# Optimization experiments

Hardware: AMD Instinct MI355X
Metric: run time of the kernel (lower is better)

Reference implementation:

```python
import jax, jax.numpy as jnp
import numpy as np

IN_DIM = 256
OUT_DIM = 256
B, N, E = 8, 1024, 262144
K_RATIO = 0.5
BN_EPS = 1e-5


def _xavier(key, shape):
    fan_in, fan_out = shape[1], shape[0]
    lim = float(np.sqrt(6.0 / (fan_in + fan_out)))
    return jax.random.uniform(key, shape, jnp.float32, -lim, lim)


def setup_inputs() -> dict:
    key = jax.random.key(0)
    ks = jax.random.split(key, 10)
    x = jax.random.normal(ks[0], (B, N, IN_DIM), jnp.float32)
    edges = jax.random.randint(ks[1], (2, E), 0, B * N, jnp.int64 if jax.config.jax_enable_x64 else jnp.int32)
    return {
        "x": x,
        "edges": edges,
        "att_proj_w": _xavier(ks[2], (OUT_DIM, IN_DIM)),
        "att_proj_b": jnp.zeros((OUT_DIM,), jnp.float32),
        "att_map_w": _xavier(ks[3], (1, OUT_DIM)).reshape(OUT_DIM),
        "pwa_w": _xavier(ks[4], (OUT_DIM, IN_DIM)),
        "pwa_b": jnp.zeros((OUT_DIM,), jnp.float32),
        "pwo_w": _xavier(ks[5], (OUT_DIM, IN_DIM)),
        "pwo_b": jnp.zeros((OUT_DIM,), jnp.float32),
        "bn_gamma": jnp.ones((OUT_DIM,), jnp.float32),
        "bn_beta": jnp.zeros((OUT_DIM,), jnp.float32),
        "y_w": _xavier(ks[6], (1, OUT_DIM)).reshape(OUT_DIM),
        "y_b": jnp.zeros((), jnp.float32),
    }


def reference(x, edges, att_proj_w, att_proj_b, att_map_w, pwa_w, pwa_b,
              pwo_w, pwo_b, bn_gamma, bn_beta, y_w, y_b):
    b, n, d = x.shape
    num_nodes = b * n
    xf = x.reshape(num_nodes, d)
    src, dst = edges[0], edges[1]  # x_j = source, x_i = destination

    # --- GAT message: alpha = att_map(tanh(att_proj(x_i * x_j))) ---
    x_j = xf[src]                                # [E, d]
    x_i = xf[dst]                                # [E, d]
    h = jnp.tanh((x_i * x_j) @ att_proj_w.T + att_proj_b)  # [E, out]
    alpha = h @ att_map_w                        # [E]

    # --- segment softmax over destination nodes ---
    amax = jax.ops.segment_max(alpha, dst, num_segments=num_nodes)
    a = jnp.exp(alpha - amax[dst])
    denom = jax.ops.segment_sum(a, dst, num_segments=num_nodes)
    w = a / (denom[dst] + 1e-16)

    # --- scatter-sum aggregate of alpha * x_j ---
    agg = jax.ops.segment_sum(w[:, None] * x_j, dst, num_segments=num_nodes)  # [num_nodes, d]

    out = agg @ pwa_w.T + pwa_b + xf @ pwo_w.T + pwo_b  # [num_nodes, out]

    # --- BatchNorm1d (training-mode batch stats, biased var) + SELU ---
    mean = out.mean(axis=0)
    var = out.var(axis=0)
    out = (out - mean) * jax.lax.rsqrt(var + BN_EPS) * bn_gamma + bn_beta
    out = jax.nn.selu(out)

    out = out.reshape(b, n, -1)  # [B, N, out]

    # --- GraphPool: top-k by sigmoid score, gate by score ---
    y = jax.nn.sigmoid(out @ y_w + y_b)  # [B, N]
    k = max(int(n * K_RATIO), 1)
    vals, ids = jax.lax.top_k(y, k)      # [B, k]
    x_top = jnp.take_along_axis(out, ids[..., None], axis=1)  # [B, k, out]
    return x_top * vals[..., None]
```

## Files before the change

### kernel.cpp

```cpp
#include <hip/hip_runtime.h>
#include <math.h>

#define NODES 8192
#define NEDGE 262144
#define DIM 256

typedef float f32x16 __attribute__((ext_vector_type(16)));
typedef _Float16 f16x8 __attribute__((ext_vector_type(8)));
typedef __fp16 h16x2 __attribute__((ext_vector_type(2)));
typedef unsigned short u16;
typedef u16 u16x8 __attribute__((ext_vector_type(8)));
typedef u16 u16x4 __attribute__((ext_vector_type(4)));

__device__ __forceinline__ float fast_tanh(float x) {
    float t = __expf(2.f * x);
    return 1.f - 2.f * __builtin_amdgcn_rcpf(t + 1.f);
}

__device__ __forceinline__ u16 h_bits(_Float16 h) {
    u16 r; __builtin_memcpy(&r, &h, 2); return r;
}

union SplitU { h16x2 h2[2]; u16x4 u4; };

__device__ __forceinline__ void split4(float p0, float p1, float p2, float p3,
                                       u16x4& v1, u16x4& v2) {
    h16x2 h01 = __builtin_amdgcn_cvt_pkrtz(p0, p1);
    h16x2 h23 = __builtin_amdgcn_cvt_pkrtz(p2, p3);
    h16x2 r01 = __builtin_amdgcn_cvt_pkrtz((p0 - (float)h01[0]) * 2048.f,
                                           (p1 - (float)h01[1]) * 2048.f);
    h16x2 r23 = __builtin_amdgcn_cvt_pkrtz((p2 - (float)h23[0]) * 2048.f,
                                           (p3 - (float)h23[1]) * 2048.f);
    SplitU c1, c2;
    c1.h2[0] = h01; c1.h2[1] = h23;
    c2.h2[0] = r01; c2.h2[1] = r23;
    v1 = c1.u4; v2 = c2.u4;
}

__global__ void k_deg(const int* __restrict__ dst, int* __restrict__ deg) {
    int e = blockIdx.x * blockDim.x + threadIdx.x;
    if (e < NEDGE) atomicAdd(&deg[dst[e]], 1);
}

__global__ void k_scan(const int* __restrict__ deg, int* __restrict__ rowptr,
                       int* __restrict__ cursor) {
    __shared__ int part[256];
    int t = threadIdx.x;
    int base = t * 32;
    int local[32];
    int s = 0;
    for (int i = 0; i < 32; ++i) { local[i] = s; s += deg[base + i]; }
    part[t] = s;
    __syncthreads();
    for (int off = 1; off < 256; off <<= 1) {
        int v = (t >= off) ? part[t - off] : 0;
        __syncthreads();
        part[t] += v;
        __syncthreads();
    }
    int excl = (t == 0) ? 0 : part[t - 1];
    for (int i = 0; i < 32; ++i) {
        int v = excl + local[i];
        rowptr[base + i] = v;
        cursor[base + i] = v;
    }
    if (t == 255) rowptr[NODES] = part[255];
}

__global__ void k_fill(const int* __restrict__ src, const int* __restrict__ dst,
                       int* __restrict__ cursor, int2* __restrict__ sdg) {
    int e = blockIdx.x * blockDim.x + threadIdx.x;
    if (e < NEDGE) {
        int pos = atomicAdd(&cursor[dst[e]], 1);
        sdg[pos] = make_int2(src[e], dst[e]);
    }
}

__global__ void k_wfrag_all(const float* __restrict__ W, const float* __restrict__ Wa,
                            const float* __restrict__ Wo, u16* __restrict__ wf,
                            u16* __restrict__ wf2) {
    int t = blockIdx.x * blockDim.x + threadIdx.x;
    const float* S;
    u16* D;
    int gks, w, mt, lane;
    if (t < 8192) {
        lane = t & 63; mt = (t >> 6) & 1; w = (t >> 7) & 3; gks = t >> 9;
        S = W; D = wf;
    } else {
        int t2 = t - 8192;
        if (t2 >= 16384) return;
        lane = t2 & 63; mt = (t2 >> 6) & 1; w = (t2 >> 7) & 3; gks = t2 >> 9;
        S = (gks < 16) ? Wa : Wo; D = wf2;
    }
    int row = w * 64 + mt * 32 + (lane & 31);
    int k0 = (gks & 15) * 16 + (lane >> 5) * 8;
    const float* p = S + (size_t)row * DIM + k0;
    u16x8 v1, v2;
#pragma unroll
    for (int j = 0; j < 8; ++j) {
        float f = p[j];
        _Float16 h1 = (_Float16)f;
        _Float16 h2 = (_Float16)((f - (float)h1) * 2048.f);
        v1[j] = h_bits(h1);
        v2[j] = h_bits(h2);
    }
    size_t base = ((size_t)(gks * 4 + w) * 4 + mt * 2) * 512 + lane * 8;
    *(u16x8*)(D + base)       = v1;
    *(u16x8*)(D + base + 512) = v2;
}

__global__ __launch_bounds__(256, 2) void k_alpha_v15(
    const float* __restrict__ x, const int2* __restrict__ sdg,
    const u16* __restrict__ wf, const float* __restrict__ bias,
    const float* __restrict__ amap, float* __restrict__ alpha_pos)
{
    __shared__ u16 p_lds[2][64][256];
    const int tid = threadIdx.x;
    const int w = tid >> 6;
    const int lane = tid & 63;
    const int l31 = lane & 31;
    const int g2 = lane >> 5;
    const int bid = blockIdx.x;
    const int wg = (bid & 7) * 512 + (bid >> 3);
    const int e0 = wg * 64;
    const int ebase = e0 + w * 16;
    const unsigned swz = ((unsigned)(l31 & 7)) << 4;

    f32x16 accM[2][2], accC[2][2];
#pragma unroll
    for (int mt = 0; mt < 2; ++mt)
#pragma unroll
        for (int nt = 0; nt < 2; ++nt) { accM[mt][nt] = (f32x16)0.f; accC[mt][nt] = (f32x16)0.f; }

    f16x8 afA[2][2], afB[2][2], afC[2][2];

#define PREFA(DST, GKS) { \
    const u16* pb_ = wf + ((size_t)((GKS) * 4 + w) * 4) * 512 + lane * 8; \
    _Pragma("unroll") for (int mt_ = 0; mt_ < 2; ++mt_) \
    _Pragma("unroll") for (int pl_ = 0; pl_ < 2; ++pl_) \
        DST[mt_][pl_] = *(const f16x8*)(const void*)(pb_ + (mt_ * 2 + pl_) * 512); }

#define KS(GKS, USE, PF) { \
    if ((GKS) + 2 < 16) { PREFA(PF, (GKS) + 2) } \
    f16x8 bfr[2][2]; \
    _Pragma("unroll") for (int nt_ = 0; nt_ < 2; ++nt_) { \
        const int en_ = nt_ * 32 + l31; \
        const unsigned off_ = ((unsigned)((GKS) * 32 + g2 * 16)) ^ swz; \
        _Pragma("unroll") for (int pl_ = 0; pl_ < 2; ++pl_) \
            bfr[nt_][pl_] = *(const f16x8*)(const void*)((const char*)&p_lds[pl_][en_][0] + off_); \
    } \
    _Pragma("unroll") for (int mt_ = 0; mt_ < 2; ++mt_) \
    _Pragma("unroll") for (int nt_ = 0; nt_ < 2; ++nt_) { \
        accM[mt_][nt_] = __builtin_amdgcn_mfma_f32_32x32x16_f16(USE[mt_][0], bfr[nt_][0], accM[mt_][nt_], 0, 0, 0); \
        accC[mt_][nt_] = __builtin_amdgcn_mfma_f32_32x32x16_f16(USE[mt_][0], bfr[nt_][1], accC[mt_][nt_], 0, 0, 0); \
        accC[mt_][nt_] = __builtin_amdgcn_mfma_f32_32x32x16_f16(USE[mt_][1], bfr[nt_][0], accC[mt_][nt_], 0, 0, 0); } }

    PREFA(afA, 0)
    PREFA(afB, 1)

#pragma unroll
    for (int i = 0; i < 16; ++i) {
        int2 sd = sdg[ebase + i];
        float4 a = *(const float4*)(x + (size_t)sd.x * DIM + lane * 4);
        float4 b = *(const float4*)(x + (size_t)sd.y * DIM + lane * 4);
        u16x4 v1, v2;
        split4(a.x * b.x, a.y * b.y, a.z * b.z, a.w * b.w, v1, v2);
        const int le = w * 16 + i;
        const unsigned off = ((unsigned)(lane * 8)) ^ (((unsigned)(le & 7)) << 4);
        *(u16x4*)((char*)&p_lds[0][le][0] + off) = v1;
        *(u16x4*)((char*)&p_lds[1][le][0] + off) = v2;
    }
    __syncthreads();

    KS(0,  afA, afC) KS(1,  afB, afA) KS(2,  afC, afB)
    KS(3,  afA, afC) KS(4,  afB, afA) KS(5,  afC, afB)
    KS(6,  afA, afC) KS(7,  afB, afA) KS(8,  afC, afB)
    KS(9,  afA, afC) KS(10, afB, afA) KS(11, afC, afB)
    KS(12, afA, afC) KS(13, afB, afA) KS(14, afC, afB)
    KS(15, afA, afC)
#undef KS
#undef PREFA

    float part[2] = {0.f, 0.f};
#pragma unroll
    for (int mt = 0; mt < 2; ++mt)
#pragma unroll
        for (int r = 0; r < 16; ++r) {
            int o = 64 * w + 32 * mt + (r & 3) + 8 * (r >> 2) + 4 * g2;
            float bo = bias[o], ao = amap[o];
#pragma unroll
            for (int nt = 0; nt < 2; ++nt) {
                float h = accM[mt][nt][r] + accC[mt][nt][r] * 4.8828125e-4f;
                part[nt] += ao * fast_tanh(h + bo);
            }
        }
    __syncthreads();
    float* red = (float*)(void*)p_lds;
#pragma unroll
    for (int nt = 0; nt < 2; ++nt) {
        float p = part[nt];
        p += __shfl_xor(p, 32);
        if (lane < 32) red[w * 64 + nt * 32 + lane] = p;
    }
    __syncthreads();
    if (tid < 64) alpha_pos[e0 + tid] = red[tid] + red[64 + tid] + red[128 + tid] + red[192 + tid];
}

__global__ void k_aggregate(
    const float* __restrict__ x, const float* __restrict__ alpha_pos,
    const int* __restrict__ rowptr, const int2* __restrict__ sdg,
    float* __restrict__ agg)
{
    int gw = (blockIdx.x * blockDim.x + threadIdx.x) >> 6;
    int lane = threadIdx.x & 63;
    if (gw >= NODES) return;
    int start = rowptr[gw], end = rowptr[gw + 1];
    int deg = end - start;
    float m = -INFINITY;
    for (int i = lane; i < deg; i += 64) m = fmaxf(m, alpha_pos[start + i]);
#pragma unroll
    for (int off = 32; off > 0; off >>= 1) m = fmaxf(m, __shfl_xor(m, off));
    float ssum = 0.f;
    for (int i = lane; i < deg; i += 64) ssum += expf(alpha_pos[start + i] - m);
#pragma unroll
    for (int off = 32; off > 0; off >>= 1) ssum += __shfl_xor(ssum, off);
    float a0 = 0.f, a1 = 0.f, a2 = 0.f, a3 = 0.f;
    int i = 0;
    for (; i + 4 <= deg; i += 4) {
        float w0 = expf(alpha_pos[start + i]     - m);
        float w1 = expf(alpha_pos[start + i + 1] - m);
        float w2 = expf(alpha_pos[start + i + 2] - m);
        float w3 = expf(alpha_pos[start + i + 3] - m);
        int r0 = sdg[start + i].x;
        int r1 = sdg[start + i + 1].x;
        int r2 = sdg[start + i + 2].x;
        int r3 = sdg[start + i + 3].x;
        float4 v0 = *(const float4*)(x + (size_t)r0 * DIM + lane * 4);
        float4 v1 = *(const float4*)(x + (size_t)r1 * DIM + lane * 4);
        float4 v2 = *(const float4*)(x + (size_t)r2 * DIM + lane * 4);
        float4 v3 = *(const float4*)(x + (size_t)r3 * DIM + lane * 4);
        a0 += w0 * v0.x + w1 * v1.x + w2 * v2.x + w3 * v3.x;
        a1 += w0 * v0.y + w1 * v1.y + w2 * v2.y + w3 * v3.y;
        a2 += w0 * v0.z + w1 * v1.z + w2 * v2.z + w3 * v3.z;
        a3 += w0 * v0.w + w1 * v1.w + w2 * v2.w + w3 * v3.w;
    }
    for (; i < deg; ++i) {
        float wgt = expf(alpha_pos[start + i] - m);
        int r = sdg[start + i].x;
        const float4 v = *(const float4*)(x + (size_t)r * DIM + lane * 4);
        a0 += wgt * v.x; a1 += wgt * v.y; a2 += wgt * v.z; a3 += wgt * v.w;
    }
    float inv = 1.f / (ssum + 1e-16f);
    float4 r; r.x = a0 * inv; r.y = a1 * inv; r.z = a2 * inv; r.w = a3 * inv;
    *(float4*)(agg + (size_t)gw * DIM + lane * 4) = r;
}

__global__ __launch_bounds__(256, 2) void k_out_mfma(
    const float* __restrict__ agg, const float* __restrict__ x,
    const u16* __restrict__ wf2, const float* __restrict__ ba,
    const float* __restrict__ bo, float* __restrict__ outb,
    float* __restrict__ psumf, float* __restrict__ psqf)
{
    __shared__ u16 p_lds[2][64][256];
    const int tid = threadIdx.x;
    const int w = tid >> 6;
    const int lane = tid & 63;
    const int l31 = lane & 31;
    const int g2 = lane >> 5;
    const int n0 = blockIdx.x * 64;
    const unsigned swz = ((unsigned)(l31 & 7)) << 4;

    f32x16 accM[2][2], accC[2][2];
#pragma unroll
    for (int mt = 0; mt < 2; ++mt)
#pragma unroll
        for (int nt = 0; nt < 2; ++nt) { accM[mt][nt] = (f32x16)0.f; accC[mt][nt] = (f32x16)0.f; }

    f16x8 afA[2][2], afB[2][2];

#define PREFA2(DST, GKS) { \
    const u16* pb_ = wf2 + ((size_t)((GKS) * 4 + w) * 4) * 512 + lane * 8; \
    _Pragma("unroll") for (int mt_ = 0; mt_ < 2; ++mt_) \
    _Pragma("unroll") for (int pl_ = 0; pl_ < 2; ++pl_) \
        DST[mt_][pl_] = *(const f16x8*)(const void*)(pb_ + (mt_ * 2 + pl_) * 512); }

#define OSTAGE(SRC) { \
    _Pragma("unroll") for (int i_ = 0; i_ < 16; ++i_) { \
        const int ln_ = w * 16 + i_; \
        float4 v_ = *(const float4*)((SRC) + (size_t)(n0 + ln_) * DIM + lane * 4); \
        u16x4 v1_, v2_; \
        split4(v_.x, v_.y, v_.z, v_.w, v1_, v2_); \
        const unsigned off_ = ((unsigned)(lane * 8)) ^ (((unsigned)(ln_ & 7)) << 4); \
        *(u16x4*)((char*)&p_lds[0][ln_][0] + off_) = v1_; \
        *(u16x4*)((char*)&p_lds[1][ln_][0] + off_) = v2_; } }

#define OKSTEP(GKS) { \
    if ((GKS) + 1 < 32) { \
        if ((GKS) & 1) { PREFA2(afA, (GKS) + 1) } else { PREFA2(afB, (GKS) + 1) } \
    } \
    f16x8 bfr[2][2]; \
    _Pragma("unroll") for (int nt_ = 0; nt_ < 2; ++nt_) { \
        const int en_ = nt_ * 32 + l31; \
        const unsigned off_ = ((unsigned)(((GKS) & 15) * 32 + g2 * 16)) ^ swz; \
        _Pragma("unroll") for (int pl_ = 0; pl_ < 2; ++pl_) \
            bfr[nt_][pl_] = *(const f16x8*)(const void*)((const char*)&p_lds[pl_][en_][0] + off_); \
    } \
    _Pragma("unroll") for (int mt_ = 0; mt_ < 2; ++mt_) \
    _Pragma("unroll") for (int nt_ = 0; nt_ < 2; ++nt_) { \
        f16x8 a1_ = ((GKS) & 1) ? afB[mt_][0] : afA[mt_][0]; \
        f16x8 a2_ = ((GKS) & 1) ? afB[mt_][1] : afA[mt_][1]; \
        accM[mt_][nt_] = __builtin_amdgcn_mfma_f32_32x32x16_f16(a1_, bfr[nt_][0], accM[mt_][nt_], 0, 0, 0); \
        accC[mt_][nt_] = __builtin_amdgcn_mfma_f32_32x32x16_f16(a1_, bfr[nt_][1], accC[mt_][nt_], 0, 0, 0); \
        accC[mt_][nt_] = __builtin_amdgcn_mfma_f32_32x32x16_f16(a2_, bfr[nt_][0], accC[mt_][nt_], 0, 0, 0); } }

    PREFA2(afA, 0)
    OSTAGE(agg)
    __syncthreads();
    OKSTEP(0)  OKSTEP(1)  OKSTEP(2)  OKSTEP(3)
    OKSTEP(4)  OKSTEP(5)  OKSTEP(6)  OKSTEP(7)
    OKSTEP(8)  OKSTEP(9)  OKSTEP(10) OKSTEP(11)
    OKSTEP(12) OKSTEP(13) OKSTEP(14) OKSTEP(15)
    __syncthreads();
    OSTAGE(x)
    __syncthreads();
    OKSTEP(16) OKSTEP(17) OKSTEP(18) OKSTEP(19)
    OKSTEP(20) OKSTEP(21) OKSTEP(22) OKSTEP(23)
    OKSTEP(24) OKSTEP(25) OKSTEP(26) OKSTEP(27)
    OKSTEP(28) OKSTEP(29) OKSTEP(30) OKSTEP(31)
#undef OSTAGE
#undef OKSTEP
#undef PREFA2

    __syncthreads();
    float* Cs = (float*)(void*)p_lds;
#pragma unroll
    for (int mt = 0; mt < 2; ++mt)
#pragma unroll
        for (int r = 0; r < 16; ++r) {
            int o = 64 * w + 32 * mt + (r & 3) + 8 * (r >> 2) + 4 * g2;
            float bs = ba[o] + bo[o];
#pragma unroll
            for (int nt = 0; nt < 2; ++nt) {
                int col = nt * 32 + l31;
                float hv = accM[mt][nt][r] + accC[mt][nt][r] * 4.8828125e-4f + bs;
                unsigned ob = ((unsigned)(col * 1024 + o * 4)) ^ (((unsigned)(col & 31)) << 4);
                *(float*)((char*)Cs + ob) = hv;
            }
        }
    __syncthreads();
    float s4[4] = {0.f, 0.f, 0.f, 0.f};
    float q4[4] = {0.f, 0.f, 0.f, 0.f};
#pragma unroll
    for (int i = 0; i < 16; ++i) {
        int ln = w * 16 + i;
        unsigned rb = ((unsigned)(ln * 1024 + lane * 16)) ^ (((unsigned)(ln & 31)) << 4);
        float4 val = *(const float4*)((const char*)Cs + rb);
        *(float4*)(outb + (size_t)(n0 + ln) * DIM + lane * 4) = val;
        s4[0] += val.x; s4[1] += val.y; s4[2] += val.z; s4[3] += val.w;
        q4[0] += val.x * val.x; q4[1] += val.y * val.y;
        q4[2] += val.z * val.z; q4[3] += val.w * val.w;
    }
    __syncthreads();
    float* rs = (float*)(void*)p_lds;
#pragma unroll
    for (int j = 0; j < 4; ++j) {
        rs[w * 256 + lane * 4 + j] = s4[j];
        rs[1024 + w * 256 + lane * 4 + j] = q4[j];
    }
    __syncthreads();
    if (tid < 256) {
        int c = tid;
        float ssum = rs[c] + rs[256 + c] + rs[512 + c] + rs[768 + c];
        float qsum = rs[1024 + c] + rs[1280 + c] + rs[1536 + c] + rs[1792 + c];
        psumf[blockIdx.x * 256 + c] = ssum;
        psqf[blockIdx.x * 256 + c] = qsum;
    }
}

__global__ void k_bnparam(const float* __restrict__ psumf, const float* __restrict__ psqf,
                          const float* __restrict__ gamma, const float* __restrict__ beta,
                          float* __restrict__ scale, float* __restrict__ shift) {
    int t = threadIdx.x;
    double s = 0.0, q = 0.0;
    for (int g = 0; g < 128; ++g) { s += (double)psumf[g * DIM + t]; q += (double)psqf[g * DIM + t]; }
    double mean = s / (double)NODES;
    double var = q / (double)NODES - mean * mean;
    float sc = (float)((double)gamma[t] / sqrt(var + 1e-5));
    scale[t] = sc;
    shift[t] = (float)((double)beta[t] - mean * (double)sc);
}

__global__ void k_bnselu(float* __restrict__ outb, const float* __restrict__ scale,
                         const float* __restrict__ shift, const float* __restrict__ yw,
                         const float* __restrict__ yb, float* __restrict__ y) {
    int gw = (blockIdx.x * blockDim.x + threadIdx.x) >> 6;
    int lane = threadIdx.x & 63;
    if (gw >= NODES) return;
    float4 v  = *(const float4*)(outb + (size_t)gw * DIM + lane * 4);
    float4 sc = *(const float4*)(scale + lane * 4);
    float4 sh = *(const float4*)(shift + lane * 4);
    const float SL = 1.0507009873554805f, SA = 1.6732632423543772f;
    float4 o;
    o.x = v.x * sc.x + sh.x;
    o.y = v.y * sc.y + sh.y;
    o.z = v.z * sc.z + sh.z;
    o.w = v.w * sc.w + sh.w;
    o.x = (o.x > 0.f) ? SL * o.x : SL * SA * expm1f(o.x);
    o.y = (o.y > 0.f) ? SL * o.y : SL * SA * expm1f(o.y);
    o.z = (o.z > 0.f) ? SL * o.z : SL * SA * expm1f(o.z);
    o.w = (o.w > 0.f) ? SL * o.w : SL * SA * expm1f(o.w);
    *(float4*)(outb + (size_t)gw * DIM + lane * 4) = o;
    float4 w = *(const float4*)(yw + lane * 4);
    float z = o.x * w.x + o.y * w.y + o.z * w.z + o.w * w.w;
#pragma unroll
    for (int off = 32; off > 0; off >>= 1) z += __shfl_xor(z, off);
    if (lane == 0) y[gw] = 1.f / (1.f + expf(-(z + yb[0])));
}

__global__ void k_topk(const float* __restrict__ y, float* __restrict__ svals,
                       int* __restrict__ sidx) {
    __shared__ float v[1024];
    __shared__ int  id[1024];
    int b = blockIdx.x, t = threadIdx.x;
    v[t] = y[b * 1024 + t];           id[t] = t;
    v[t + 512] = y[b * 1024 + t + 512]; id[t + 512] = t + 512;
    __syncthreads();
    for (int k = 2; k <= 1024; k <<= 1) {
        for (int j = k >> 1; j > 0; j >>= 1) {
            for (int i = t; i < 1024; i += 512) {
                int l = i ^ j;
                if (l > i) {
                    float vi = v[i], vl = v[l];
                    int ii = id[i], il = id[l];
                    bool precede = (vi > vl) || (vi == vl && ii < il);
                    bool dirDesc = ((i & k) == 0);
                    bool sw = dirDesc ? !precede : precede;
                    if (sw) { v[i] = vl; v[l] = vi; id[i] = il; id[l] = ii; }
                }
            }
            __syncthreads();
        }
    }
    if (t < 512) { svals[b * 512 + t] = v[t]; sidx[b * 512 + t] = id[t]; }
}

__global__ void k_gather(const float* __restrict__ outb, const float* __restrict__ svals,
                         const int* __restrict__ sidx, float* __restrict__ dout) {
    int gw = (blockIdx.x * blockDim.x + threadIdx.x) >> 6;
    int lane = threadIdx.x & 63;
    int b = gw >> 9, r = gw & 511;
    float val = svals[b * 512 + r];
    int idn = sidx[b * 512 + r];
    float4 vv = *(const float4*)(outb + (size_t)(b * 1024 + idn) * DIM + lane * 4);
    vv.x *= val; vv.y *= val; vv.z *= val; vv.w *= val;
    *(float4*)(dout + (size_t)(b * 512 + r) * DIM + lane * 4) = vv;
}

extern "C" void kernel_launch(void* const* d_in, const int* in_sizes, int n_in,
                              void* d_out, int out_size, void* d_ws, size_t ws_size,
                              hipStream_t stream) {
    const float* x     = (const float*)d_in[0];
    const int* edges   = (const int*)d_in[1];
    const float* att_w = (const float*)d_in[2];
    const float* att_b = (const float*)d_in[3];
    const float* amap  = (const float*)d_in[4];
    const float* pwa_w = (const float*)d_in[5];
    const float* pwa_b = (const float*)d_in[6];
    const float* pwo_w = (const float*)d_in[7];
    const float* pwo_b = (const float*)d_in[8];
    const float* gamma = (const float*)d_in[9];
    const float* beta  = (const float*)d_in[10];
    const float* yw    = (const float*)d_in[11];
    const float* yb    = (const float*)d_in[12];
    float* out = (float*)d_out;
    const int* src = edges;
    const int* dst = edges + NEDGE;

    char* ws = (char*)d_ws;
    size_t off = 0;
    auto alloc = [&](size_t b) { void* p = ws + off; off = (off + b + 255) & ~(size_t)255; return p; };
    float* alpha  = (float*)alloc((size_t)NEDGE * 4);
    int2*  sdg    = (int2*)alloc((size_t)NEDGE * 8);
    float* agg    = (float*)alloc((size_t)NODES * DIM * 4);
    float* outb   = (float*)alloc((size_t)NODES * DIM * 4);
    int*   deg    = (int*)alloc(NODES * 4);
    int*   rowptr = (int*)alloc((NODES + 1) * 4);
    int*   cursor = (int*)alloc(NODES * 4);
    float* psumf  = (float*)alloc(128 * DIM * 4);
    float* psqf   = (float*)alloc(128 * DIM * 4);
    float* scale  = (float*)alloc(DIM * 4);
    float* shift  = (float*)alloc(DIM * 4);
    float* yv     = (float*)alloc(NODES * 4);
    float* svals  = (float*)alloc(8 * 512 * 4);
    int*   sidx   = (int*)alloc(8 * 512 * 4);
    u16*   wf     = (u16*)alloc((size_t)16 * 4 * 4 * 512 * 2);
    u16*   wf2    = (u16*)alloc((size_t)32 * 4 * 4 * 512 * 2);

    (void)hipMemsetAsync(deg, 0, NODES * 4, stream);
    k_wfrag_all<<<96, 256, 0, stream>>>(att_w, pwa_w, pwo_w, wf, wf2);
    k_deg<<<NEDGE / 256, 256, 0, stream>>>(dst, deg);
    k_scan<<<1, 256, 0, stream>>>(deg, rowptr, cursor);
    k_fill<<<NEDGE / 256, 256, 0, stream>>>(src, dst, cursor, sdg);
    k_alpha_v15<<<NEDGE / 64, 256, 0, stream>>>(x, sdg, wf, att_b, amap, alpha);
    k_aggregate<<<NODES / 4, 256, 0, stream>>>(x, alpha, rowptr, sdg, agg);
    k_out_mfma<<<NODES / 64, 256, 0, stream>>>(agg, x, wf2, pwa_b, pwo_b, outb, psumf, psqf);
    k_bnparam<<<1, 256, 0, stream>>>(psumf, psqf, gamma, beta, scale, shift);
    k_bnselu<<<NODES / 4, 256, 0, stream>>>(outb, scale, shift, yw, yb, yv);
    k_topk<<<8, 512, 0, stream>>>(yv, svals, sidx);
    k_gather<<<(8 * 512) / 4, 256, 0, stream>>>(outb, svals, sidx, out);
}
```

Before: 258.1 us.

## Fuse degree count into weight prep, sort segments, shrink GEMM tile, widen top-k

Merges the degree-count atomics into the weight-fragment kernel to save a launch. Adds an edge-id array and a per-node insertion sort so each segment keeps original edge order, making the sum order deterministic. Halves the output GEMM tile to 32 nodes per block so twice as many blocks run, which doubles the BN partial-sum rows. Runs the top-k bitonic sort with 1024 threads instead of 512. The extra sort kernel adds serial per-thread work and memory traffic.

```diff
diff --git a/kernel.cpp b/kernel.cpp
--- a/kernel.cpp
+++ b/kernel.cpp
@@ -37,11 +37,6 @@
     v1 = c1.u4; v2 = c2.u4;
 }
 
-__global__ void k_deg(const int* __restrict__ dst, int* __restrict__ deg) {
-    int e = blockIdx.x * blockDim.x + threadIdx.x;
-    if (e < NEDGE) atomicAdd(&deg[dst[e]], 1);
-}
-
 __global__ void k_scan(const int* __restrict__ deg, int* __restrict__ rowptr,
                        int* __restrict__ cursor) {
     __shared__ int part[256];
@@ -68,18 +63,45 @@
 }
 
 __global__ void k_fill(const int* __restrict__ src, const int* __restrict__ dst,
-                       int* __restrict__ cursor, int2* __restrict__ sdg) {
+                       int* __restrict__ cursor, int2* __restrict__ sdg,
+                       int* __restrict__ eid) {
     int e = blockIdx.x * blockDim.x + threadIdx.x;
     if (e < NEDGE) {
         int pos = atomicAdd(&cursor[dst[e]], 1);
         sdg[pos] = make_int2(src[e], dst[e]);
-    }
-}
-
-__global__ void k_wfrag_all(const float* __restrict__ W, const float* __restrict__ Wa,
+        eid[pos] = e;
+    }
+}
+
+__global__ void k_sortseg(const int* __restrict__ rowptr, int* __restrict__ eid,
+                          int2* __restrict__ sdg) {
+    int n = blockIdx.x * blockDim.x + threadIdx.x;
+    if (n >= NODES) return;
+    int s = rowptr[n], e = rowptr[n + 1];
+    for (int i = s + 1; i < e; ++i) {
+        int key = eid[i];
+        int2 kv = sdg[i];
+        int j = i - 1;
+        while (j >= s && eid[j] > key) {
+            eid[j + 1] = eid[j];
+            sdg[j + 1] = sdg[j];
+            --j;
+        }
+        eid[j + 1] = key;
+        sdg[j + 1] = kv;
+    }
+}
+
+__global__ void k_wfrag_deg(const float* __restrict__ W, const float* __restrict__ Wa,
                             const float* __restrict__ Wo, u16* __restrict__ wf,
-                            u16* __restrict__ wf2) {
-    int t = blockIdx.x * blockDim.x + threadIdx.x;
+                            u16* __restrict__ wf2, const int* __restrict__ dst,
+                            int* __restrict__ deg) {
+    if (blockIdx.x >= 96) {
+        int e = (blockIdx.x - 96) * 256 + threadIdx.x;
+        if (e < NEDGE) atomicAdd(&deg[dst[e]], 1);
+        return;
+    }
+    int t = blockIdx.x * 256 + threadIdx.x;
     const float* S;
     u16* D;
     int gks, w, mt, lane;
@@ -88,7 +110,6 @@
         S = W; D = wf;
     } else {
         int t2 = t - 8192;
-        if (t2 >= 16384) return;
         lane = t2 & 63; mt = (t2 >> 6) & 1; w = (t2 >> 7) & 3; gks = t2 >> 9;
         S = (gks < 16) ? Wa : Wo; D = wf2;
     }
@@ -261,20 +282,18 @@
     const float* __restrict__ bo, float* __restrict__ outb,
     float* __restrict__ psumf, float* __restrict__ psqf)
 {
-    __shared__ u16 p_lds[2][64][256];
+    __shared__ u16 p_lds[2][32][256];
     const int tid = threadIdx.x;
     const int w = tid >> 6;
     const int lane = tid & 63;
     const int l31 = lane & 31;
     const int g2 = lane >> 5;
-    const int n0 = blockIdx.x * 64;
+    const int n0 = blockIdx.x * 32;
     const unsigned swz = ((unsigned)(l31 & 7)) << 4;
 
-    f32x16 accM[2][2], accC[2][2];
-#pragma unroll
-    for (int mt = 0; mt < 2; ++mt)
-#pragma unroll
-        for (int nt = 0; nt < 2; ++nt) { accM[mt][nt] = (f32x16)0.f; accC[mt][nt] = (f32x16)0.f; }
+    f32x16 accM[2], accC[2];
+#pragma unroll
+    for (int mt = 0; mt < 2; ++mt) { accM[mt] = (f32x16)0.f; accC[mt] = (f32x16)0.f; }
 
     f16x8 afA[2][2], afB[2][2];
 
@@ -285,8 +304,8 @@
         DST[mt_][pl_] = *(const f16x8*)(const void*)(pb_ + (mt_ * 2 + pl_) * 512); }
 
 #define OSTAGE(SRC) { \
-    _Pragma("unroll") for (int i_ = 0; i_ < 16; ++i_) { \
-        const int ln_ = w * 16 + i_; \
+    _Pragma("unroll") for (int i_ = 0; i_ < 8; ++i_) { \
+        const int ln_ = w * 8 + i_; \
         float4 v_ = *(const float4*)((SRC) + (size_t)(n0 + ln_) * DIM + lane * 4); \
         u16x4 v1_, v2_; \
         split4(v_.x, v_.y, v_.z, v_.w, v1_, v2_); \
@@ -298,20 +317,18 @@
     if ((GKS) + 1 < 32) { \
         if ((GKS) & 1) { PREFA2(afA, (GKS) + 1) } else { PREFA2(afB, (GKS) + 1) } \
     } \
-    f16x8 bfr[2][2]; \
-    _Pragma("unroll") for (int nt_ = 0; nt_ < 2; ++nt_) { \
-        const int en_ = nt_ * 32 + l31; \
+    f16x8 bfr[2]; \
+    { \
         const unsigned off_ = ((unsigned)(((GKS) & 15) * 32 + g2 * 16)) ^ swz; \
         _Pragma("unroll") for (int pl_ = 0; pl_ < 2; ++pl_) \
-            bfr[nt_][pl_] = *(const f16x8*)(const void*)((const char*)&p_lds[pl_][en_][0] + off_); \
+            bfr[pl_] = *(const f16x8*)(const void*)((const char*)&p_lds[pl_][l31][0] + off_); \
     } \
-    _Pragma("unroll") for (int mt_ = 0; mt_ < 2; ++mt_) \
-    _Pragma("unroll") for (int nt_ = 0; nt_ < 2; ++nt_) { \
+    _Pragma("unroll") for (int mt_ = 0; mt_ < 2; ++mt_) { \
         f16x8 a1_ = ((GKS) & 1) ? afB[mt_][0] : afA[mt_][0]; \
         f16x8 a2_ = ((GKS) & 1) ? afB[mt_][1] : afA[mt_][1]; \
-        accM[mt_][nt_] = __builtin_amdgcn_mfma_f32_32x32x16_f16(a1_, bfr[nt_][0], accM[mt_][nt_], 0, 0, 0); \
-        accC[mt_][nt_] = __builtin_amdgcn_mfma_f32_32x32x16_f16(a1_, bfr[nt_][1], accC[mt_][nt_], 0, 0, 0); \
-        accC[mt_][nt_] = __builtin_amdgcn_mfma_f32_32x32x16_f16(a2_, bfr[nt_][0], accC[mt_][nt_], 0, 0, 0); } }
+        accM[mt_] = __builtin_amdgcn_mfma_f32_32x32x16_f16(a1_, bfr[0], accM[mt_], 0, 0, 0); \
+        accC[mt_] = __builtin_amdgcn_mfma_f32_32x32x16_f16(a1_, bfr[1], accC[mt_], 0, 0, 0); \
+        accC[mt_] = __builtin_amdgcn_mfma_f32_32x32x16_f16(a2_, bfr[0], accC[mt_], 0, 0, 0); } }
 
     PREFA2(afA, 0)
     OSTAGE(agg)
@@ -339,20 +356,17 @@
         for (int r = 0; r < 16; ++r) {
             int o = 64 * w + 32 * mt + (r & 3) + 8 * (r >> 2) + 4 * g2;
             float bs = ba[o] + bo[o];
-#pragma unroll
-            for (int nt = 0; nt < 2; ++nt) {
-                int col = nt * 32 + l31;
-                float hv = accM[mt][nt][r] + accC[mt][nt][r] * 4.8828125e-4f + bs;
-                unsigned ob = ((unsigned)(col * 1024 + o * 4)) ^ (((unsigned)(col & 31)) << 4);
-                *(float*)((char*)Cs + ob) = hv;
-            }
+            int col = l31;
+            float hv = accM[mt][r] + accC[mt][r] * 4.8828125e-4f + bs;
+            unsigned ob = ((unsigned)(col * 1024 + o * 4)) ^ (((unsigned)(col & 31)) << 4);
+            *(float*)((char*)Cs + ob) = hv;
         }
     __syncthreads();
     float s4[4] = {0.f, 0.f, 0.f, 0.f};
     float q4[4] = {0.f, 0.f, 0.f, 0.f};
 #pragma unroll
-    for (int i = 0; i < 16; ++i) {
-        int ln = w * 16 + i;
+    for (int i = 0; i < 8; ++i) {
+        int ln = w * 8 + i;
         unsigned rb = ((unsigned)(ln * 1024 + lane * 16)) ^ (((unsigned)(ln & 31)) << 4);
         float4 val = *(const float4*)((const char*)Cs + rb);
         *(float4*)(outb + (size_t)(n0 + ln) * DIM + lane * 4) = val;
@@ -382,7 +396,7 @@
                           float* __restrict__ scale, float* __restrict__ shift) {
     int t = threadIdx.x;
     double s = 0.0, q = 0.0;
-    for (int g = 0; g < 128; ++g) { s += (double)psumf[g * DIM + t]; q += (double)psqf[g * DIM + t]; }
+    for (int g = 0; g < 256; ++g) { s += (double)psumf[g * DIM + t]; q += (double)psqf[g * DIM + t]; }
     double mean = s / (double)NODES;
     double var = q / (double)NODES - mean * mean;
     float sc = (float)((double)gamma[t] / sqrt(var + 1e-5));
@@ -422,21 +436,19 @@
     __shared__ float v[1024];
     __shared__ int  id[1024];
     int b = blockIdx.x, t = threadIdx.x;
-    v[t] = y[b * 1024 + t];           id[t] = t;
-    v[t + 512] = y[b * 1024 + t + 512]; id[t + 512] = t + 512;
+    v[t] = y[b * 1024 + t];
+    id[t] = t;
     __syncthreads();
     for (int k = 2; k <= 1024; k <<= 1) {
         for (int j = k >> 1; j > 0; j >>= 1) {
-            for (int i = t; i < 1024; i += 512) {
-                int l = i ^ j;
-                if (l > i) {
-                    float vi = v[i], vl = v[l];
-                    int ii = id[i], il = id[l];
-                    bool precede = (vi > vl) || (vi == vl && ii < il);
-                    bool dirDesc = ((i & k) == 0);
-                    bool sw = dirDesc ? !precede : precede;
-                    if (sw) { v[i] = vl; v[l] = vi; id[i] = il; id[l] = ii; }
-                }
+            int l = t ^ j;
+            if (l > t) {
+                float vt = v[t], vl = v[l];
+                int it = id[t], il = id[l];
+                bool precede = (vt > vl) || (vt == vl && it < il);
+                bool dirDesc = ((t & k) == 0);
+                bool sw = dirDesc ? !precede : precede;
+                if (sw) { v[t] = vl; v[l] = vt; id[t] = il; id[l] = it; }
             }
             __syncthreads();
         }
@@ -481,13 +493,14 @@
     auto alloc = [&](size_t b) { void* p = ws + off; off = (off + b + 255) & ~(size_t)255; return p; };
     float* alpha  = (float*)alloc((size_t)NEDGE * 4);
     int2*  sdg    = (int2*)alloc((size_t)NEDGE * 8);
+    int*   eid    = (int*)alloc((size_t)NEDGE * 4);
     float* agg    = (float*)alloc((size_t)NODES * DIM * 4);
     float* outb   = (float*)alloc((size_t)NODES * DIM * 4);
     int*   deg    = (int*)alloc(NODES * 4);
     int*   rowptr = (int*)alloc((NODES + 1) * 4);
     int*   cursor = (int*)alloc(NODES * 4);
-    float* psumf  = (float*)alloc(128 * DIM * 4);
-    float* psqf   = (float*)alloc(128 * DIM * 4);
+    float* psumf  = (float*)alloc(256 * DIM * 4);
+    float* psqf   = (float*)alloc(256 * DIM * 4);
     float* scale  = (float*)alloc(DIM * 4);
     float* shift  = (float*)alloc(DIM * 4);
     float* yv     = (float*)alloc(NODES * 4);
@@ -497,15 +510,15 @@
     u16*   wf2    = (u16*)alloc((size_t)32 * 4 * 4 * 512 * 2);
 
     (void)hipMemsetAsync(deg, 0, NODES * 4, stream);
-    k_wfrag_all<<<96, 256, 0, stream>>>(att_w, pwa_w, pwo_w, wf, wf2);
-    k_deg<<<NEDGE / 256, 256, 0, stream>>>(dst, deg);
+    k_wfrag_deg<<<96 + NEDGE / 256, 256, 0, stream>>>(att_w, pwa_w, pwo_w, wf, wf2, dst, deg);
     k_scan<<<1, 256, 0, stream>>>(deg, rowptr, cursor);
-    k_fill<<<NEDGE / 256, 256, 0, stream>>>(src, dst, cursor, sdg);
+    k_fill<<<NEDGE / 256, 256, 0, stream>>>(src, dst, cursor, sdg, eid);
+    k_sortseg<<<NODES / 256, 256, 0, stream>>>(rowptr, eid, sdg);
     k_alpha_v15<<<NEDGE / 64, 256, 0, stream>>>(x, sdg, wf, att_b, amap, alpha);
     k_aggregate<<<NODES / 4, 256, 0, stream>>>(x, alpha, rowptr, sdg, agg);
-    k_out_mfma<<<NODES / 64, 256, 0, stream>>>(agg, x, wf2, pwa_b, pwo_b, outb, psumf, psqf);
+    k_out_mfma<<<NODES / 32, 256, 0, stream>>>(agg, x, wf2, pwa_b, pwo_b, outb, psumf, psqf);
     k_bnparam<<<1, 256, 0, stream>>>(psumf, psqf, gamma, beta, scale, shift);
     k_bnselu<<<NODES / 4, 256, 0, stream>>>(outb, scale, shift, yw, yb, yv);
-    k_topk<<<8, 512, 0, stream>>>(yv, svals, sidx);
+    k_topk<<<8, 1024, 0, stream>>>(yv, svals, sidx);
     k_gather<<<(8 * 512) / 4, 256, 0, stream>>>(outb, svals, sidx, out);
 }
```

Measured after the change: 542.6 us. 2.1x slower.
